# Kernel tuning notes

Measured on AMD Instinct MI355X. Metric: run time of the kernel, lower is better.

The kernel has to match this reference:

```python
import jax, jax.numpy as jnp
import numpy as np

N_NODES = 100000
N_EDGES = 1600000
EDGE_DIM = 32
NODE_DIM = 128
GLOBAL_DIM = 32
HIDDEN = 256


def setup_inputs() -> dict:
    key = jax.random.key(0)
    ks = jax.random.split(key, 8)
    edge_attrs = jax.random.normal(ks[0], (N_EDGES, EDGE_DIM), dtype=jnp.float32)
    senders = jax.random.randint(ks[1], (N_EDGES,), 0, N_NODES, dtype=jnp.int32)
    receivers = jax.random.randint(ks[2], (N_EDGES,), 0, N_NODES, dtype=jnp.int32)
    node_attrs = jax.random.normal(ks[3], (N_NODES, NODE_DIM), dtype=jnp.float32)
    global_attrs = jax.random.normal(ks[4], (GLOBAL_DIM,), dtype=jnp.float32)
    in_dim = 2 * EDGE_DIM + NODE_DIM + GLOBAL_DIM  # 224
    W1 = jax.random.normal(ks[5], (in_dim, HIDDEN), dtype=jnp.float32) * (1.0 / np.sqrt(in_dim))
    b1 = jnp.zeros((HIDDEN,), dtype=jnp.float32)
    W2 = jax.random.normal(ks[6], (HIDDEN, NODE_DIM), dtype=jnp.float32) * (1.0 / np.sqrt(HIDDEN))
    b2 = jnp.zeros((NODE_DIM,), dtype=jnp.float32)
    return {
        "edge_attrs": edge_attrs,
        "senders": senders,
        "receivers": receivers,
        "node_attrs": node_attrs,
        "global_attrs": global_attrs,
        "W1": W1,
        "b1": b1,
        "W2": W2,
        "b2": b2,
    }


def reference(edge_attrs, senders, receivers, node_attrs, global_attrs, W1, b1, W2, b2):
    n_nodes = node_attrs.shape[0]
    # Aggregate (sum) edge attributes of incoming edges per node.
    rec_agg = jax.ops.segment_sum(edge_attrs, receivers, num_segments=n_nodes)
    # Aggregate (sum) edge attributes of outgoing edges per node.
    send_agg = jax.ops.segment_sum(edge_attrs, senders, num_segments=n_nodes)
    # Broadcast global attributes to every node and concat features.
    glob = jnp.broadcast_to(global_attrs[None, :], (n_nodes, global_attrs.shape[0]))
    feats = jnp.concatenate([rec_agg, send_agg, node_attrs, glob], axis=-1)  # [N, 224]
    # Node-attribute update function: 2-layer MLP with ReLU.
    h = jax.nn.relu(feats @ W1 + b1)
    new_node_attrs = h @ W2 + b2  # [N, NODE_DIM]
    return new_node_attrs
```

## Files before the change

kernel.cpp:

```cpp
#include <hip/hip_runtime.h>

#define N_NODES   100000
#define N_EDGES   1600000
#define EDGE_DIM  32
#define NODE_DIM  128
#define K1        192
#define HIDDEN    256
#define OUT_DIM   128
#define NCNT      (2 * N_NODES)
#define SCAN_BLK  1024
#define NSCAN     ((NCNT + SCAN_BLK - 1) / SCAN_BLK)

#define RSHIFT  10
#define NRANGES 98
#define NBKT    (2 * NRANGES)
#define SBLK    4096
#define NSBLK   ((N_EDGES + SBLK - 1) / SBLK)

typedef float  f32x4   __attribute__((ext_vector_type(4)));
typedef short  short8  __attribute__((ext_vector_type(8)));
typedef unsigned short ushort8 __attribute__((ext_vector_type(8)));
typedef unsigned short ushort4v __attribute__((ext_vector_type(4)));

#define W_BIN    0
#define W_EIDS   3200000
#define W_FEATS  6400000
#define W_W1T    9600000
#define W_W2T    (W_W1T + 24576)
#define W_B1E    (W_W2T + 16384)
#define W_OFF    (W_B1E + 256)
#define W_BCNT   (W_OFF + NCNT + 1)
#define W_BBASE  (W_BCNT + 256)
#define W_BCUR   (W_BBASE + 256)
#define W_TOTAL  (W_BCUR + 256)

#define S_FEATS_W  0
#define S_W1T_W    3200000
#define S_W2T_W    (S_W1T_W + 24576)
#define S_B1E_W    (S_W2T_W + 16384)
#define S_CNT_W    (S_B1E_W + 256)
#define S_OFF_W    (S_CNT_W + NCNT)
#define S_POS_W    (S_OFF_W + NCNT + 1)
#define S_EIDS_W   (S_POS_W + NCNT + 1)
#define S_BSUM_W   (S_EIDS_W + 2 * N_EDGES)

__device__ __forceinline__ unsigned short f2bf(float f) {
    unsigned int u = __float_as_uint(f);
    return (unsigned short)((u + 0x7fffu + ((u >> 16) & 1u)) >> 16);
}

__global__ __launch_bounds__(256) void wcvt_kernel(
    const float* __restrict__ W1, const float* __restrict__ W2,
    const float* __restrict__ b1, const float* __restrict__ glob,
    unsigned short* __restrict__ W1T, unsigned short* __restrict__ W2T,
    float* __restrict__ b1e)
{
    int id = blockIdx.x * 256 + threadIdx.x;
    if (id < K1 * HIDDEN) {
        int n = id / K1, k = id - n * K1;
        W1T[id] = f2bf(W1[(size_t)k * HIDDEN + n]);
    } else if (id < K1 * HIDDEN + HIDDEN * OUT_DIM) {
        int id2 = id - K1 * HIDDEN;
        int o = id2 / HIDDEN, k = id2 - o * HIDDEN;
        W2T[id2] = f2bf(W2[(size_t)k * OUT_DIM + o]);
    } else if (id < K1 * HIDDEN + HIDDEN * OUT_DIM + HIDDEN) {
        int n = id - (K1 * HIDDEN + HIDDEN * OUT_DIM);
        float s = b1[n];
        #pragma unroll
        for (int j = 0; j < 32; ++j)
            s += glob[j] * W1[(size_t)(K1 + j) * HIDDEN + n];
        b1e[n] = s;
    }
}

__global__ __launch_bounds__(512) void bin_count_kernel(
    const int* __restrict__ rcv, const int* __restrict__ snd,
    int* __restrict__ bcnt)
{
    __shared__ int h[NBKT];
    const int tid = threadIdx.x;
    for (int i = tid; i < NBKT; i += 512) h[i] = 0;
    __syncthreads();

    const int base = blockIdx.x * SBLK;
    #pragma unroll
    for (int k = 0; k < SBLK / 512; ++k) {
        int e = base + k * 512 + tid;
        if (e < N_EDGES) {
            atomicAdd(&h[rcv[e] >> RSHIFT], 1);
            atomicAdd(&h[NRANGES + (snd[e] >> RSHIFT)], 1);
        }
    }
    __syncthreads();
    for (int i = tid; i < NBKT; i += 512)
        if (h[i]) atomicAdd(&bcnt[i], h[i]);
}

__global__ __launch_bounds__(256) void scan196_kernel(
    const int* __restrict__ bcnt, int* __restrict__ bbase, int* __restrict__ bcur,
    int* __restrict__ off)
{
    __shared__ int ts[256];
    const int t = threadIdx.x;
    int v = (t < NBKT) ? bcnt[t] : 0;
    ts[t] = v;
    __syncthreads();
    for (int d = 1; d < 256; d <<= 1) {
        int x = (t >= d) ? ts[t - d] : 0;
        __syncthreads();
        ts[t] += x;
        __syncthreads();
    }
    if (t < NBKT) { int ex = ts[t] - v; bbase[t] = ex; bcur[t] = ex; }
    if (t == 255) { bbase[NBKT] = ts[255]; off[NCNT] = 2 * N_EDGES; }
}

__global__ __launch_bounds__(512) void bin_scatter_ids_kernel(
    const int* __restrict__ rcv, const int* __restrict__ snd,
    int*         __restrict__ bcur,
    unsigned int* __restrict__ bin)
{
    __shared__ int cntA[NBKT];
    __shared__ int baseS[NBKT];
    __shared__ int cntC[NBKT];

    const int tid  = threadIdx.x;
    const int base = blockIdx.x * SBLK;

    for (int i = tid; i < NBKT; i += 512) { cntA[i] = 0; cntC[i] = 0; }
    __syncthreads();

    int rk[SBLK / 512], sk[SBLK / 512];
    #pragma unroll
    for (int k = 0; k < SBLK / 512; ++k) {
        int e = base + k * 512 + tid;
        if (e < N_EDGES) {
            rk[k] = rcv[e]; sk[k] = snd[e];
            atomicAdd(&cntA[rk[k] >> RSHIFT], 1);
            atomicAdd(&cntA[NRANGES + (sk[k] >> RSHIFT)], 1);
        } else rk[k] = -1;
    }
    __syncthreads();

    for (int i = tid; i < NBKT; i += 512)
        baseS[i] = cntA[i] ? atomicAdd(&bcur[i], cntA[i]) : 0;
    __syncthreads();

    #pragma unroll
    for (int k = 0; k < SBLK / 512; ++k) {
        if (rk[k] < 0) continue;
        int e  = base + k * 512 + tid;
        int b0 = rk[k] >> RSHIFT;
        int b1 = NRANGES + (sk[k] >> RSHIFT);
        int s0 = baseS[b0] + atomicAdd(&cntC[b0], 1);
        int s1 = baseS[b1] + atomicAdd(&cntC[b1], 1);
        bin[s0] = ((unsigned)(rk[k] & ((1 << RSHIFT) - 1)) << 21) | (unsigned)e;
        bin[s1] = ((unsigned)(sk[k] & ((1 << RSHIFT) - 1)) << 21) | (unsigned)e;
    }
}

__global__ __launch_bounds__(1024) void bucket_fill_kernel(
    const unsigned int* __restrict__ bin,
    const int* __restrict__ bbase,
    int* __restrict__ off,
    int* __restrict__ eids)
{
    __shared__ int hist[1024];
    __shared__ int ts[1024];
    __shared__ int cur[1024];

    const int tid = threadIdx.x;
    const int b   = blockIdx.x;
    const int dir = (b >= NRANGES) ? 1 : 0;
    const int r   = dir ? (b - NRANGES) : b;
    const int lo  = r << RSHIFT;
    const int s0  = bbase[b], s1 = bbase[b + 1];

    hist[tid] = 0;
    __syncthreads();

    for (int i = s0 + tid; i < s1; i += 1024)
        atomicAdd(&hist[bin[i] >> 21], 1);
    __syncthreads();

    int v = hist[tid];
    ts[tid] = v;
    __syncthreads();
    for (int d = 1; d < 1024; d <<= 1) {
        int x = (tid >= d) ? ts[tid - d] : 0;
        __syncthreads();
        ts[tid] += x;
        __syncthreads();
    }
    int slot0 = s0 + ts[tid] - v;
    cur[tid] = slot0;

    const int rangeN = min(1024, N_NODES - lo);
    if (tid < rangeN) off[dir * N_NODES + lo + tid] = slot0;
    __syncthreads();

    for (int i = s0 + tid; i < s1; i += 1024) {
        unsigned int u = bin[i];
        int nl = u >> 21;
        int s = atomicAdd(&cur[nl], 1);
        eids[s] = (int)(u & 0x1FFFFFu);
    }
}

__global__ __launch_bounds__(256) void gather_kernel(
    const float* __restrict__ edge,
    const int*   __restrict__ off,
    const int*   __restrict__ eids,
    unsigned short* __restrict__ feats_bf)
{
    int seg = blockIdx.x * 32 + (threadIdx.x >> 3);
    if (seg >= NCNT) return;
    const int sub = threadIdx.x & 7;
    int s = off[seg], e = off[seg + 1];
    float4 a = make_float4(0.f, 0.f, 0.f, 0.f);
    for (int i = s; i < e; ++i) {
        int eid = eids[i];
        float4 v = *(const float4*)&edge[(size_t)eid * EDGE_DIM + sub * 4];
        a.x += v.x; a.y += v.y; a.z += v.z; a.w += v.w;
    }
    int nodeI = (seg < N_NODES) ? seg : (seg - N_NODES);
    int colB  = (seg < N_NODES) ? 0 : 32;
    ushort4v r;
    r.x = f2bf(a.x); r.y = f2bf(a.y); r.z = f2bf(a.z); r.w = f2bf(a.w);
    *(ushort4v*)&feats_bf[(size_t)nodeI * 64 + colB + sub * 4] = r;
}

__global__ __launch_bounds__(256) void hist_kernel(
    const int* __restrict__ snd, const int* __restrict__ rcv, int* __restrict__ cnt)
{
    int e = blockIdx.x * 256 + threadIdx.x;
    if (e >= N_EDGES) return;
    atomicAdd(&cnt[rcv[e]], 1);
    atomicAdd(&cnt[N_NODES + snd[e]], 1);
}

__global__ __launch_bounds__(256) void scan1_kernel(
    const int* __restrict__ cnt, int* __restrict__ off, int* __restrict__ bsum)
{
    __shared__ int ts[256];
    const int t = threadIdx.x;
    const int base = blockIdx.x * SCAN_BLK + t * 4;
    int v[4], s = 0;
    #pragma unroll
    for (int j = 0; j < 4; ++j) {
        int idx = base + j;
        v[j] = (idx < NCNT) ? cnt[idx] : 0;
        s += v[j];
    }
    ts[t] = s;
    __syncthreads();
    for (int d = 1; d < 256; d <<= 1) {
        int x = (t >= d) ? ts[t - d] : 0;
        __syncthreads();
        ts[t] += x;
        __syncthreads();
    }
    int run = ts[t] - s;
    #pragma unroll
    for (int j = 0; j < 4; ++j) {
        int idx = base + j;
        if (idx < NCNT) off[idx] = run;
        run += v[j];
    }
    if (t == 255) bsum[blockIdx.x] = ts[255];
}

__global__ __launch_bounds__(256) void scan23_kernel(
    int* __restrict__ off, const int* __restrict__ bsum, int* __restrict__ pos)
{
    __shared__ int ts[256];
    __shared__ int sboff;
    const int t = threadIdx.x;
    int v = (t < NSCAN) ? bsum[t] : 0;
    ts[t] = v;
    __syncthreads();
    for (int d = 1; d < 256; d <<= 1) {
        int x = (t >= d) ? ts[t - d] : 0;
        __syncthreads();
        ts[t] += x;
        __syncthreads();
    }
    if (t == (int)blockIdx.x) sboff = ts[t] - v;
    __syncthreads();
    const int bo = sboff;
    const int base = blockIdx.x * SCAN_BLK + t * 4;
    #pragma unroll
    for (int j = 0; j < 4; ++j) {
        int idx = base + j;
        if (idx < NCNT) {
            int o = off[idx] + bo;
            off[idx] = o;
            pos[idx] = o;
        }
    }
    if (blockIdx.x == 0 && t == 0) off[NCNT] = 2 * N_EDGES;
}

__global__ __launch_bounds__(256) void fill_kernel(
    const int* __restrict__ snd, const int* __restrict__ rcv,
    int* __restrict__ pos, int* __restrict__ eids)
{
    int e = blockIdx.x * 256 + threadIdx.x;
    if (e >= N_EDGES) return;
    int p = atomicAdd(&pos[rcv[e]], 1);
    eids[p] = e;
    int q = atomicAdd(&pos[N_NODES + snd[e]], 1);
    eids[q] = e;
}

__global__ __launch_bounds__(512) void gemm12_kernel(
    const unsigned short* __restrict__ feats_bf,
    const float* __restrict__ node,
    const unsigned short* __restrict__ W1T,
    const float* __restrict__ b1e,
    const unsigned short* __restrict__ W2T,
    const float* __restrict__ b2,
    float*       __restrict__ out)
{
    __shared__ unsigned short sA[64 * K1];
    __shared__ unsigned short sH[64 * HIDDEN];

    const int tid  = threadIdx.x;
    const int base = blockIdx.x * 64;

    for (int idx = tid; idx < 64 * 24; idx += 512) {
        int row = idx / 24;
        int c   = idx - row * 24;
        int g   = base + row; if (g >= N_NODES) g = N_NODES - 1;
        ushort8 r;
        if (c < 8) {
            r = *(const ushort8*)&feats_bf[(size_t)g * 64 + c * 8];
        } else {
            const float* np = &node[(size_t)g * NODE_DIM + (c - 8) * 8];
            float4 v0 = *(const float4*)np;
            float4 v1 = *(const float4*)(np + 4);
            r[0] = f2bf(v0.x); r[1] = f2bf(v0.y); r[2] = f2bf(v0.z); r[3] = f2bf(v0.w);
            r[4] = f2bf(v1.x); r[5] = f2bf(v1.y); r[6] = f2bf(v1.z); r[7] = f2bf(v1.w);
        }
        *(ushort8*)&sA[row * K1 + ((c ^ (row & 7)) << 3)] = r;
    }
    __syncthreads();

    const int wave = tid >> 6;
    const int lane = tid & 63;
    const int lm   = lane & 15;
    const int lk   = lane >> 4;

    short8 w1f[2][6];
    #pragma unroll
    for (int j = 0; j < 2; ++j) {
        int nt = 2 * wave + j;
        #pragma unroll
        for (int k = 0; k < 6; ++k)
            w1f[j][k] = *(const short8*)&W1T[(size_t)(nt * 16 + lm) * K1 + k * 32 + lk * 8];
    }

    f32x4 acc1[4][2];
    {
        float bv0 = b1e[(2 * wave) * 16 + lm];
        float bv1 = b1e[(2 * wave + 1) * 16 + lm];
        #pragma unroll
        for (int m = 0; m < 4; ++m) {
            acc1[m][0] = (f32x4){bv0, bv0, bv0, bv0};
            acc1[m][1] = (f32x4){bv1, bv1, bv1, bv1};
        }
    }

    #pragma unroll
    for (int k = 0; k < 6; ++k) {
        #pragma unroll
        for (int m = 0; m < 4; ++m) {
            int row   = m * 16 + lm;
            int chunk = k * 4 + lk;
            short8 af = *(const short8*)&sA[row * K1 + ((chunk ^ (row & 7)) << 3)];
            acc1[m][0] = __builtin_amdgcn_mfma_f32_16x16x32_bf16(af, w1f[0][k], acc1[m][0], 0, 0, 0);
            acc1[m][1] = __builtin_amdgcn_mfma_f32_16x16x32_bf16(af, w1f[1][k], acc1[m][1], 0, 0, 0);
        }
    }

    #pragma unroll
    for (int m = 0; m < 4; ++m) {
        #pragma unroll
        for (int j = 0; j < 2; ++j) {
            int col   = (2 * wave + j) * 16 + lm;
            int chunk = col >> 3;
            int cin   = col & 7;
            #pragma unroll
            for (int r = 0; r < 4; ++r) {
                int rowl = m * 16 + lk * 4 + r;
                float v = fmaxf(acc1[m][j][r], 0.0f);
                sH[rowl * HIDDEN + ((chunk ^ (rowl & 7)) << 3) + cin] = f2bf(v);
            }
        }
    }

    short8 w2f[8];
    #pragma unroll
    for (int k = 0; k < 8; ++k)
        w2f[k] = *(const short8*)&W2T[(size_t)(wave * 16 + lm) * HIDDEN + k * 32 + lk * 8];

    f32x4 acc2[4];
    {
        float bv = b2[wave * 16 + lm];
        #pragma unroll
        for (int m = 0; m < 4; ++m) acc2[m] = (f32x4){bv, bv, bv, bv};
    }
    __syncthreads();

    #pragma unroll
    for (int k = 0; k < 8; ++k) {
        #pragma unroll
        for (int m = 0; m < 4; ++m) {
            int row   = m * 16 + lm;
            int chunk = k * 4 + lk;
            short8 hf = *(const short8*)&sH[row * HIDDEN + ((chunk ^ (row & 7)) << 3)];
            acc2[m] = __builtin_amdgcn_mfma_f32_16x16x32_bf16(hf, w2f[k], acc2[m], 0, 0, 0);
        }
    }

    #pragma unroll
    for (int m = 0; m < 4; ++m) {
        #pragma unroll
        for (int r = 0; r < 4; ++r) {
            int grow = base + m * 16 + lk * 4 + r;
            if (grow < N_NODES)
                out[(size_t)grow * OUT_DIM + wave * 16 + lm] = acc2[m][r];
        }
    }
}

extern "C" void kernel_launch(void* const* d_in, const int* in_sizes, int n_in,
                              void* d_out, int out_size, void* d_ws, size_t ws_size,
                              hipStream_t stream) {
    const float* edge = (const float*)d_in[0];
    const int*   snd  = (const int*)  d_in[1];
    const int*   rcv  = (const int*)  d_in[2];
    const float* node = (const float*)d_in[3];
    const float* glob = (const float*)d_in[4];
    const float* W1   = (const float*)d_in[5];
    const float* b1   = (const float*)d_in[6];
    const float* W2   = (const float*)d_in[7];
    const float* b2   = (const float*)d_in[8];
    float* out = (float*)d_out;

    int* wsi = (int*)d_ws;
    const int wblocks = (K1 * HIDDEN + HIDDEN * OUT_DIM + HIDDEN + 255) / 256;

    if (ws_size >= (size_t)W_TOTAL * 4) {
        unsigned int*   bin      = (unsigned int*)(wsi + W_BIN);
        int*            eids     = wsi + W_EIDS;
        unsigned short* feats_bf = (unsigned short*)(wsi + W_FEATS);
        unsigned short* W1T      = (unsigned short*)(wsi + W_W1T);
        unsigned short* W2T      = (unsigned short*)(wsi + W_W2T);
        float*          b1e      = (float*)(wsi + W_B1E);
        int* off   = wsi + W_OFF;
        int* bcnt  = wsi + W_BCNT;
        int* bbase = wsi + W_BBASE;
        int* bcur  = wsi + W_BCUR;

        hipMemsetAsync(bcnt, 0, NBKT * sizeof(int), stream);
        wcvt_kernel          <<<wblocks, 256, 0, stream>>>(W1, W2, b1, glob, W1T, W2T, b1e);
        bin_count_kernel     <<<NSBLK, 512, 0, stream>>>(rcv, snd, bcnt);
        scan196_kernel       <<<1, 256, 0, stream>>>(bcnt, bbase, bcur, off);
        bin_scatter_ids_kernel<<<NSBLK, 512, 0, stream>>>(rcv, snd, bcur, bin);
        bucket_fill_kernel   <<<NBKT, 1024, 0, stream>>>(bin, bbase, off, eids);
        gather_kernel        <<<(NCNT + 31) / 32, 256, 0, stream>>>(edge, off, eids, feats_bf);
        gemm12_kernel<<<(N_NODES + 63) / 64, 512, 0, stream>>>(
            feats_bf, node, W1T, b1e, W2T, b2, out);
    } else {
        unsigned short* feats_bf = (unsigned short*)(wsi + S_FEATS_W);
        unsigned short* W1T      = (unsigned short*)(wsi + S_W1T_W);
        unsigned short* W2T      = (unsigned short*)(wsi + S_W2T_W);
        float*          b1e      = (float*)(wsi + S_B1E_W);
        int* cnt  = wsi + S_CNT_W;
        int* off  = wsi + S_OFF_W;
        int* pos  = wsi + S_POS_W;
        int* eids = wsi + S_EIDS_W;
        int* bsum = wsi + S_BSUM_W;

        hipMemsetAsync(cnt, 0, NCNT * sizeof(int), stream);
        wcvt_kernel  <<<wblocks, 256, 0, stream>>>(W1, W2, b1, glob, W1T, W2T, b1e);
        const int eblocks = (N_EDGES + 255) / 256;
        hist_kernel  <<<eblocks, 256, 0, stream>>>(snd, rcv, cnt);
        scan1_kernel <<<NSCAN,   256, 0, stream>>>(cnt, off, bsum);
        scan23_kernel<<<NSCAN,   256, 0, stream>>>(off, bsum, pos);
        fill_kernel  <<<eblocks, 256, 0, stream>>>(snd, rcv, pos, eids);
        gather_kernel<<<(NCNT + 31) / 32, 256, 0, stream>>>(edge, off, eids, feats_bf);
        gemm12_kernel<<<(N_NODES + 63) / 64, 512, 0, stream>>>(
            feats_bf, node, W1T, b1e, W2T, b2, out);
    }
}
```

Before: 228.1 us.

## Retile fused MLP waves to 2x4 fragments and unroll gather by two

The fused GEMM kernel now splits its 8 waves into 2 row halves by 4 column quarters instead of giving each wave all 64 rows. This halves the shared-memory A/H fragment reads per wave at the cost of more W1/W2 fragment loads from global memory. W1 fragments are loaded per k-step rather than all held at once, and launch bounds now request 4 blocks per CU, which constrains register use. The gather loop is unrolled by two with a second accumulator so two edge loads are in flight at once, which also changes the float summation order.

Result: slower. 243.2 us (+6.6%).

```diff
diff --git a/kernel.cpp b/kernel.cpp
--- a/kernel.cpp
+++ b/kernel.cpp
@@ -217,12 +217,23 @@
     if (seg >= NCNT) return;
     const int sub = threadIdx.x & 7;
     int s = off[seg], e = off[seg + 1];
-    float4 a = make_float4(0.f, 0.f, 0.f, 0.f);
-    for (int i = s; i < e; ++i) {
-        int eid = eids[i];
-        float4 v = *(const float4*)&edge[(size_t)eid * EDGE_DIM + sub * 4];
+
+    float4 a  = make_float4(0.f, 0.f, 0.f, 0.f);
+    float4 a2 = make_float4(0.f, 0.f, 0.f, 0.f);
+    int i = s;
+    for (; i + 2 <= e; i += 2) {
+        int e0 = eids[i], e1 = eids[i + 1];
+        float4 v0 = *(const float4*)&edge[(size_t)e0 * EDGE_DIM + sub * 4];
+        float4 v1 = *(const float4*)&edge[(size_t)e1 * EDGE_DIM + sub * 4];
+        a.x  += v0.x; a.y  += v0.y; a.z  += v0.z; a.w  += v0.w;
+        a2.x += v1.x; a2.y += v1.y; a2.z += v1.z; a2.w += v1.w;
+    }
+    if (i < e) {
+        float4 v = *(const float4*)&edge[(size_t)eids[i] * EDGE_DIM + sub * 4];
         a.x += v.x; a.y += v.y; a.z += v.z; a.w += v.w;
     }
+    a.x += a2.x; a.y += a2.y; a.z += a2.z; a.w += a2.w;
+
     int nodeI = (seg < N_NODES) ? seg : (seg - N_NODES);
     int colB  = (seg < N_NODES) ? 0 : 32;
     ushort4v r;
@@ -313,7 +324,7 @@
     eids[q] = e;
 }
 
-__global__ __launch_bounds__(512) void gemm12_kernel(
+__global__ __launch_bounds__(512, 4) void gemm12_kernel(
     const unsigned short* __restrict__ feats_bf,
     const float* __restrict__ node,
     const unsigned short* __restrict__ W1T,
@@ -350,86 +361,89 @@
     const int lane = tid & 63;
     const int lm   = lane & 15;
     const int lk   = lane >> 4;
-
-    short8 w1f[2][6];
-    #pragma unroll
-    for (int j = 0; j < 2; ++j) {
-        int nt = 2 * wave + j;
-        #pragma unroll
-        for (int k = 0; k < 6; ++k)
-            w1f[j][k] = *(const short8*)&W1T[(size_t)(nt * 16 + lm) * K1 + k * 32 + lk * 8];
-    }
-
-    f32x4 acc1[4][2];
-    {
-        float bv0 = b1e[(2 * wave) * 16 + lm];
-        float bv1 = b1e[(2 * wave + 1) * 16 + lm];
-        #pragma unroll
-        for (int m = 0; m < 4; ++m) {
-            acc1[m][0] = (f32x4){bv0, bv0, bv0, bv0};
-            acc1[m][1] = (f32x4){bv1, bv1, bv1, bv1};
-        }
+    const int mh   = wave >> 2;
+    const int nq   = wave & 3;
+
+    f32x4 acc1[2][4];
+    #pragma unroll
+    for (int j = 0; j < 4; ++j) {
+        float bv = b1e[(nq * 4 + j) * 16 + lm];
+        acc1[0][j] = (f32x4){bv, bv, bv, bv};
+        acc1[1][j] = (f32x4){bv, bv, bv, bv};
     }
 
     #pragma unroll
     for (int k = 0; k < 6; ++k) {
-        #pragma unroll
-        for (int m = 0; m < 4; ++m) {
-            int row   = m * 16 + lm;
+        short8 w1f[4];
+        #pragma unroll
+        for (int j = 0; j < 4; ++j)
+            w1f[j] = *(const short8*)&W1T[(size_t)((nq * 4 + j) * 16 + lm) * K1 + k * 32 + lk * 8];
+        #pragma unroll
+        for (int m = 0; m < 2; ++m) {
+            int row   = (mh * 2 + m) * 16 + lm;
             int chunk = k * 4 + lk;
             short8 af = *(const short8*)&sA[row * K1 + ((chunk ^ (row & 7)) << 3)];
-            acc1[m][0] = __builtin_amdgcn_mfma_f32_16x16x32_bf16(af, w1f[0][k], acc1[m][0], 0, 0, 0);
-            acc1[m][1] = __builtin_amdgcn_mfma_f32_16x16x32_bf16(af, w1f[1][k], acc1[m][1], 0, 0, 0);
-        }
-    }
-
-    #pragma unroll
-    for (int m = 0; m < 4; ++m) {
-        #pragma unroll
-        for (int j = 0; j < 2; ++j) {
-            int col   = (2 * wave + j) * 16 + lm;
+            #pragma unroll
+            for (int j = 0; j < 4; ++j)
+                acc1[m][j] = __builtin_amdgcn_mfma_f32_16x16x32_bf16(af, w1f[j], acc1[m][j], 0, 0, 0);
+        }
+    }
+
+    #pragma unroll
+    for (int m = 0; m < 2; ++m) {
+        #pragma unroll
+        for (int j = 0; j < 4; ++j) {
+            int col   = (nq * 4 + j) * 16 + lm;
             int chunk = col >> 3;
             int cin   = col & 7;
             #pragma unroll
             for (int r = 0; r < 4; ++r) {
-                int rowl = m * 16 + lk * 4 + r;
+                int rowl = (mh * 2 + m) * 16 + lk * 4 + r;
                 float v = fmaxf(acc1[m][j][r], 0.0f);
                 sH[rowl * HIDDEN + ((chunk ^ (rowl & 7)) << 3) + cin] = f2bf(v);
             }
         }
     }
 
-    short8 w2f[8];
+    short8 w2f[8][2];
     #pragma unroll
     for (int k = 0; k < 8; ++k)
-        w2f[k] = *(const short8*)&W2T[(size_t)(wave * 16 + lm) * HIDDEN + k * 32 + lk * 8];
-
-    f32x4 acc2[4];
-    {
-        float bv = b2[wave * 16 + lm];
-        #pragma unroll
-        for (int m = 0; m < 4; ++m) acc2[m] = (f32x4){bv, bv, bv, bv};
+        #pragma unroll
+        for (int j2 = 0; j2 < 2; ++j2)
+            w2f[k][j2] = *(const short8*)&W2T[(size_t)((nq * 2 + j2) * 16 + lm) * HIDDEN + k * 32 + lk * 8];
+
+    f32x4 acc2[2][2];
+    #pragma unroll
+    for (int j2 = 0; j2 < 2; ++j2) {
+        float bv = b2[(nq * 2 + j2) * 16 + lm];
+        acc2[0][j2] = (f32x4){bv, bv, bv, bv};
+        acc2[1][j2] = (f32x4){bv, bv, bv, bv};
     }
     __syncthreads();
 
     #pragma unroll
     for (int k = 0; k < 8; ++k) {
         #pragma unroll
-        for (int m = 0; m < 4; ++m) {
-            int row   = m * 16 + lm;
+        for (int m = 0; m < 2; ++m) {
+            int row   = (mh * 2 + m) * 16 + lm;
             int chunk = k * 4 + lk;
             short8 hf = *(const short8*)&sH[row * HIDDEN + ((chunk ^ (row & 7)) << 3)];
-            acc2[m] = __builtin_amdgcn_mfma_f32_16x16x32_bf16(hf, w2f[k], acc2[m], 0, 0, 0);
-        }
-    }
-
-    #pragma unroll
-    for (int m = 0; m < 4; ++m) {
-        #pragma unroll
-        for (int r = 0; r < 4; ++r) {
-            int grow = base + m * 16 + lk * 4 + r;
-            if (grow < N_NODES)
-                out[(size_t)grow * OUT_DIM + wave * 16 + lm] = acc2[m][r];
+            #pragma unroll
+            for (int j2 = 0; j2 < 2; ++j2)
+                acc2[m][j2] = __builtin_amdgcn_mfma_f32_16x16x32_bf16(hf, w2f[k][j2], acc2[m][j2], 0, 0, 0);
+        }
+    }
+
+    #pragma unroll
+    for (int m = 0; m < 2; ++m) {
+        #pragma unroll
+        for (int j2 = 0; j2 < 2; ++j2) {
+            #pragma unroll
+            for (int r = 0; r < 4; ++r) {
+                int grow = base + (mh * 2 + m) * 16 + lk * 4 + r;
+                if (grow < N_NODES)
+                    out[(size_t)grow * OUT_DIM + (nq * 2 + j2) * 16 + lm] = acc2[m][j2][r];
+            }
         }
     }
 }
```
